# Performance work log

Hardware: AMD Instinct MI355X
Metric: run time of the kernel (lower is better)

Reference implementation:

```python
import jax, jax.numpy as jnp
import numpy as np

# Larq ste_sign: forward sign(x) with sign(0)=+1; backward is identity clipped to |x|<=1 (STE).
@jax.custom_vjp
def ste_sign(x):
    return jnp.where(x >= 0, jnp.ones((), x.dtype), -jnp.ones((), x.dtype))

def _ste_fwd(x):
    return ste_sign(x), x

def _ste_bwd(x, g):
    return (g * (jnp.abs(x) <= 1).astype(g.dtype),)

ste_sign.defvjp(_ste_fwd, _ste_bwd)


def setup_inputs() -> dict:
    key = jax.random.key(0)
    k1, k2 = jax.random.split(key)
    x = jax.random.normal(k1, (16, 112, 112, 256), dtype=jnp.float32)      # NHWC
    kernel = jax.random.normal(k2, (3, 3, 256, 1), dtype=jnp.float32) * 0.1  # (kh, kw, C, mult)
    return {"x": x, "kernel": kernel}


def reference(x, kernel):
    # Quantize input and depthwise kernel, then standard depthwise conv (stride 1, SAME, no bias).
    xq = ste_sign(x)
    kq = ste_sign(kernel)
    kh, kw, C, mult = kernel.shape
    rhs = kq.reshape(kh, kw, 1, C * mult)  # HWIO layout for grouped conv
    out = jax.lax.conv_general_dilated(
        xq, rhs,
        window_strides=(1, 1),
        padding="SAME",
        feature_group_count=C,
        dimension_numbers=("NHWC", "HWIO", "NHWC"),
    )
    return out
```

## Files before the change

### kernel.cpp

```cpp
#include <hip/hip_runtime.h>


constexpr int N = 16, H = 112, W = 112, C = 256;
constexpr int TW = 28;

struct I4 { int v[4]; };

__device__ __forceinline__ I4 load4i(const float* p) {
    const int4 t = *reinterpret_cast<const int4*>(p);
    I4 r; r.v[0] = t.x; r.v[1] = t.y; r.v[2] = t.z; r.v[3] = t.w;
    return r;
}

template<bool TOP, bool BOT>
__device__ __forceinline__ void run_strip(
        const float* __restrict__ x, const float* __restrict__ k,
        float* __restrict__ out, int n, int h, int w0, int c0) {

    constexpr int NROWS = 1 + (TOP ? 1 : 0) + (BOT ? 1 : 0);

    int km[3][3][4];
#pragma unroll
    for (int r = 0; r < 3; ++r)
#pragma unroll
        for (int j = 0; j < 3; ++j) {
            const int4 kv = *reinterpret_cast<const int4*>(k + (r * 3 + j) * C + c0);
            km[r][j][0] = kv.x >> 31; km[r][j][1] = kv.y >> 31;
            km[r][j][2] = kv.z >> 31; km[r][j][3] = kv.w >> 31;
        }

    const size_t rowstride = (size_t)W * C;
    const float* rc = x + (size_t)(n * H + h) * rowstride + c0;
    const float* rm = rc - rowstride;
    const float* rp = rc + rowstride;
    float* orow = out + (size_t)(n * H + h) * rowstride + c0;

    auto colD = [&](int cc, int dj[3][4]) {
        I4 xm, xc, xp;
        if (TOP) xm = load4i(rm + (size_t)cc * C);
        xc = load4i(rc + (size_t)cc * C);
        if (BOT) xp = load4i(rp + (size_t)cc * C);
#pragma unroll
        for (int ch = 0; ch < 4; ++ch) {
            const int am = TOP ? (xm.v[ch] >> 31) : 0;
            const int ac = xc.v[ch] >> 31;
            const int ap = BOT ? (xp.v[ch] >> 31) : 0;
#pragma unroll
            for (int j = 0; j < 3; ++j) {
                int s = ac ^ km[1][j][ch];
                if (TOP) s += am ^ km[0][j][ch];
                if (BOT) s += ap ^ km[2][j][ch];
                dj[j][ch] = NROWS + 2 * s;
            }
        }
    };

    int d0_m2[4], d0_m1[4], d1_m1[4];

    if (w0 > 0) {
        int dj[3][4]; colD(w0 - 1, dj);
#pragma unroll
        for (int ch = 0; ch < 4; ++ch) d0_m2[ch] = dj[0][ch];
    } else {
#pragma unroll
        for (int ch = 0; ch < 4; ++ch) d0_m2[ch] = 0;
    }
    {
        int dj[3][4]; colD(w0, dj);
#pragma unroll
        for (int ch = 0; ch < 4; ++ch) { d0_m1[ch] = dj[0][ch]; d1_m1[ch] = dj[1][ch]; }
    }

#pragma unroll 3
    for (int i = 1; i < TW; ++i) {
        const int cc = w0 + i;
        int dj[3][4]; colD(cc, dj);
        float ov[4];
#pragma unroll
        for (int ch = 0; ch < 4; ++ch) {
            ov[ch] = (float)(d0_m2[ch] + d1_m1[ch] + dj[2][ch]);
            d0_m2[ch] = d0_m1[ch]; d0_m1[ch] = dj[0][ch]; d1_m1[ch] = dj[1][ch];
        }
        *reinterpret_cast<float4*>(orow + (size_t)(cc - 1) * C) =
            make_float4(ov[0], ov[1], ov[2], ov[3]);
    }

    {
        const int cc = w0 + TW;
        int d2v[4] = {0, 0, 0, 0};
        if (cc < W) {
            int dj[3][4]; colD(cc, dj);
#pragma unroll
            for (int ch = 0; ch < 4; ++ch) d2v[ch] = dj[2][ch];
        }
        float ov[4];
#pragma unroll
        for (int ch = 0; ch < 4; ++ch) ov[ch] = (float)(d0_m2[ch] + d1_m1[ch] + d2v[ch]);
        *reinterpret_cast<float4*>(orow + (size_t)(cc - 1) * C) =
            make_float4(ov[0], ov[1], ov[2], ov[3]);
    }
}

__global__ __launch_bounds__(256) void bsign_dw3x3_strip(
        const float* __restrict__ x, const float* __restrict__ k,
        float* __restrict__ out) {
    const int c0 = (threadIdx.x & 63) << 2;
    const int wq = threadIdx.x >> 6;
    const int h  = blockIdx.y * 4 + wq;
    const int w0 = blockIdx.x * TW;
    const int n  = blockIdx.z;

    if (h == 0)            run_strip<false, true >(x, k, out, n, h, w0, c0);
    else if (h == H - 1)   run_strip<true,  false>(x, k, out, n, h, w0, c0);
    else                   run_strip<true,  true >(x, k, out, n, h, w0, c0);
}

extern "C" void kernel_launch(void* const* d_in, const int* in_sizes, int n_in,
                              void* d_out, int out_size, void* d_ws, size_t ws_size,
                              hipStream_t stream) {
    const float* x = (const float*)d_in[0];
    const float* k = (const float*)d_in[1];
    float* out = (float*)d_out;

    dim3 grid(W / TW, H / 4, N);
    bsign_dw3x3_strip<<<grid, 256, 0, stream>>>(x, k, out);
}
```

Before: 384.2 us.

## Use bit-packed popcount for sign dot products, nontemporal stores, narrower strips

```diff
diff --git a/kernel.cpp b/kernel.cpp
--- a/kernel.cpp
+++ b/kernel.cpp
@@ -2,32 +2,33 @@
 
 
 constexpr int N = 16, H = 112, W = 112, C = 256;
-constexpr int TW = 28;
+constexpr int TW = 16;
 
-struct I4 { int v[4]; };
-
-__device__ __forceinline__ I4 load4i(const float* p) {
-    const int4 t = *reinterpret_cast<const int4*>(p);
-    I4 r; r.v[0] = t.x; r.v[1] = t.y; r.v[2] = t.z; r.v[3] = t.w;
-    return r;
-}
+typedef float f32x4 __attribute__((ext_vector_type(4)));
 
 template<bool TOP, bool BOT>
 __device__ __forceinline__ void run_strip(
         const float* __restrict__ x, const float* __restrict__ k,
         float* __restrict__ out, int n, int h, int w0, int c0) {
 
-    constexpr int NROWS = 1 + (TOP ? 1 : 0) + (BOT ? 1 : 0);
+    constexpr unsigned VMASK = (TOP ? 0x1u : 0u) | 0x8u | (BOT ? 0x40u : 0u);
+    constexpr int NROWS = (TOP ? 1 : 0) + 1 + (BOT ? 1 : 0);
 
-    int km[3][3][4];
+    unsigned kb[4] = {0u, 0u, 0u, 0u};
 #pragma unroll
-    for (int r = 0; r < 3; ++r)
+    for (int t = 0; t < 9; ++t) {
+        const uint4 kv = *reinterpret_cast<const uint4*>(k + t * C + c0);
+        kb[0] |= (kv.x >> 31) << t;
+        kb[1] |= (kv.y >> 31) << t;
+        kb[2] |= (kv.z >> 31) << t;
+        kb[3] |= (kv.w >> 31) << t;
+    }
+    unsigned kbj[3][4];
 #pragma unroll
-        for (int j = 0; j < 3; ++j) {
-            const int4 kv = *reinterpret_cast<const int4*>(k + (r * 3 + j) * C + c0);
-            km[r][j][0] = kv.x >> 31; km[r][j][1] = kv.y >> 31;
-            km[r][j][2] = kv.z >> 31; km[r][j][3] = kv.w >> 31;
-        }
+    for (int j = 0; j < 3; ++j)
+#pragma unroll
+        for (int ch = 0; ch < 4; ++ch)
+            kbj[j][ch] = (kb[ch] >> j) & 0x49u & VMASK;
 
     const size_t rowstride = (size_t)W * C;
     const float* rc = x + (size_t)(n * H + h) * rowstride + c0;
@@ -36,23 +37,27 @@
     float* orow = out + (size_t)(n * H + h) * rowstride + c0;
 
     auto colD = [&](int cc, int dj[3][4]) {
-        I4 xm, xc, xp;
-        if (TOP) xm = load4i(rm + (size_t)cc * C);
-        xc = load4i(rc + (size_t)cc * C);
-        if (BOT) xp = load4i(rp + (size_t)cc * C);
+        uint4 xm = make_uint4(0,0,0,0), xp = make_uint4(0,0,0,0);
+        if constexpr (TOP) xm = *reinterpret_cast<const uint4*>(rm + (size_t)cc * C);
+        const uint4 xc = *reinterpret_cast<const uint4*>(rc + (size_t)cc * C);
+        if constexpr (BOT) xp = *reinterpret_cast<const uint4*>(rp + (size_t)cc * C);
+
+        unsigned xcode[4];
+        {
+            const unsigned* m = &xm.x; const unsigned* c = &xc.x; const unsigned* p = &xp.x;
 #pragma unroll
-        for (int ch = 0; ch < 4; ++ch) {
-            const int am = TOP ? (xm.v[ch] >> 31) : 0;
-            const int ac = xc.v[ch] >> 31;
-            const int ap = BOT ? (xp.v[ch] >> 31) : 0;
-#pragma unroll
-            for (int j = 0; j < 3; ++j) {
-                int s = ac ^ km[1][j][ch];
-                if (TOP) s += am ^ km[0][j][ch];
-                if (BOT) s += ap ^ km[2][j][ch];
-                dj[j][ch] = NROWS + 2 * s;
+            for (int ch = 0; ch < 4; ++ch) {
+                unsigned r = (c[ch] >> 31) << 3;
+                if constexpr (TOP) r |= (m[ch] >> 31);
+                if constexpr (BOT) r |= (p[ch] >> 31) << 6;
+                xcode[ch] = r;
             }
         }
+#pragma unroll
+        for (int ch = 0; ch < 4; ++ch)
+#pragma unroll
+            for (int j = 0; j < 3; ++j)
+                dj[j][ch] = NROWS - 2 * __popc(xcode[ch] ^ kbj[j][ch]);
     };
 
     int d0_m2[4], d0_m1[4], d1_m1[4];
@@ -75,14 +80,14 @@
     for (int i = 1; i < TW; ++i) {
         const int cc = w0 + i;
         int dj[3][4]; colD(cc, dj);
-        float ov[4];
+        f32x4 ov;
 #pragma unroll
         for (int ch = 0; ch < 4; ++ch) {
             ov[ch] = (float)(d0_m2[ch] + d1_m1[ch] + dj[2][ch]);
             d0_m2[ch] = d0_m1[ch]; d0_m1[ch] = dj[0][ch]; d1_m1[ch] = dj[1][ch];
         }
-        *reinterpret_cast<float4*>(orow + (size_t)(cc - 1) * C) =
-            make_float4(ov[0], ov[1], ov[2], ov[3]);
+        __builtin_nontemporal_store(ov,
+            reinterpret_cast<f32x4*>(orow + (size_t)(cc - 1) * C));
     }
 
     {
@@ -93,15 +98,15 @@
 #pragma unroll
             for (int ch = 0; ch < 4; ++ch) d2v[ch] = dj[2][ch];
         }
-        float ov[4];
+        f32x4 ov;
 #pragma unroll
         for (int ch = 0; ch < 4; ++ch) ov[ch] = (float)(d0_m2[ch] + d1_m1[ch] + d2v[ch]);
-        *reinterpret_cast<float4*>(orow + (size_t)(cc - 1) * C) =
-            make_float4(ov[0], ov[1], ov[2], ov[3]);
+        __builtin_nontemporal_store(ov,
+            reinterpret_cast<f32x4*>(orow + (size_t)(cc - 1) * C));
     }
 }
 
-__global__ __launch_bounds__(256) void bsign_dw3x3_strip(
+__global__ __launch_bounds__(256) void bsign_dw3x3_pop(
         const float* __restrict__ x, const float* __restrict__ k,
         float* __restrict__ out) {
     const int c0 = (threadIdx.x & 63) << 2;
@@ -123,5 +128,5 @@
     float* out = (float*)d_out;
 
     dim3 grid(W / TW, H / 4, N);
-    bsign_dw3x3_strip<<<grid, 256, 0, stream>>>(x, k, out);
+    bsign_dw3x3_pop<<<grid, 256, 0, stream>>>(x, k, out);
 }
```

Measured after the change: 350.8 us. 8.7% less time.
